# Optimization experiments

Hardware: AMD Instinct MI355X
Metric: run time of the kernel (lower is better)

Reference implementation:

```python
import jax, jax.numpy as jnp
import numpy as np

N_NODES = 50000
N_EDGES = 800000
F_IN = 64
HID = 64
N_GRAPHS = 256
BN_EPS = 1e-5


def setup_inputs() -> dict:
    key = jax.random.key(0)
    ks = jax.random.split(key, 16)
    inp = {
        'x': jax.random.normal(ks[0], (N_NODES, F_IN), dtype=jnp.float32),
        'edge_index': jax.random.randint(ks[1], (2, N_EDGES), 0, N_NODES, dtype=jnp.int64),
        'edge_weight': jax.random.uniform(ks[2], (N_EDGES,), dtype=jnp.float32),
        'batch': jnp.sort(jax.random.randint(ks[3], (N_NODES,), 0, N_GRAPHS, dtype=jnp.int64)),
    }
    def lin(k, fi, fo):
        s = 1.0 / np.sqrt(fi)
        kw, kb = jax.random.split(k)
        return (jax.random.uniform(kw, (fi, fo), jnp.float32, -s, s),
                jax.random.uniform(kb, (fo,), jnp.float32, -s, s))
    inp['W1'], inp['b1'] = lin(ks[4], F_IN, HID)
    inp['W2'], inp['b2'] = lin(ks[5], HID, HID)
    inp['W3'], inp['b3'] = lin(ks[6], HID, HID)
    inp['fcW1'], inp['fcb1'] = lin(ks[7], HID, HID)
    inp['fcW2'], inp['fcb2'] = lin(ks[8], HID, 1)
    for i, k in zip((1, 2, 3), ks[9:12]):
        inp[f'g{i}'] = jnp.ones((HID,), jnp.float32)
        inp[f'be{i}'] = jnp.zeros((HID,), jnp.float32)
    return inp


def gin_conv(x, src, dst, edge_weight, W, b):
    # weighted scatter-add aggregation: agg[dst] += w_e * x[src]
    msg = x[src] * edge_weight[:, None]            # [E, d]
    agg = jax.ops.segment_sum(msg, dst, num_segments=x.shape[0])  # [N, d]
    return (x + agg) @ W + b                       # GIN eps=0, nn = Linear


def batch_norm(x, gamma, beta):
    mu = jnp.mean(x, axis=0)
    var = jnp.var(x, axis=0)
    return (x - mu) * jax.lax.rsqrt(var + BN_EPS) * gamma + beta


def reference(x, edge_index, edge_weight, batch,
              W1, b1, W2, b2, W3, b3, fcW1, fcb1, fcW2, fcb2,
              g1, be1, g2, be2, g3, be3):
    src, dst = edge_index[0], edge_index[1]
    h = batch_norm(jax.nn.relu(gin_conv(x, src, dst, edge_weight, W1, b1)), g1, be1)
    h = batch_norm(jax.nn.relu(gin_conv(h, src, dst, edge_weight, W2, b2)), g2, be2)
    h = batch_norm(gin_conv(h, src, dst, edge_weight, W3, b3), g3, be3)
    pooled = jax.ops.segment_sum(h, batch, num_segments=N_GRAPHS)  # global_add_pool
    h = jax.nn.relu(pooled)
    h = jax.nn.relu(h @ fcW1 + fcb1)
    # dropout is identity in eval / deterministic reference
    return (h @ fcW2 + fcb2).reshape(-1)
```

## Files before the change

### kernel.cpp

```cpp
#include <hip/hip_runtime.h>
#include <hip/hip_bf16.h>


#define NN 50000
#define NE 800000
#define FD 64
#define NG 256
#define CAP 64
#define BN_EPS 1e-5f

__device__ __forceinline__ float4 dec4(uint2 a) {
    float4 f;
    f.x = __uint_as_float(a.x << 16);
    f.y = __uint_as_float(a.x & 0xFFFF0000u);
    f.z = __uint_as_float(a.y << 16);
    f.w = __uint_as_float(a.y & 0xFFFF0000u);
    return f;
}
__device__ __forceinline__ unsigned rbf(float f) {
    unsigned u = __float_as_uint(f);
    return (u + 0x7FFFu + ((u >> 16) & 1u)) >> 16;
}
__device__ __forceinline__ uint2 enc4(float4 v) {
    uint2 o;
    o.x = rbf(v.x) | (rbf(v.y) << 16);
    o.y = rbf(v.z) | (rbf(v.w) << 16);
    return o;
}

__global__ __launch_bounds__(256) void build_slots_kernel(
    const int* __restrict__ src, const int* __restrict__ dst,
    const float* __restrict__ ew, int* __restrict__ cursor,
    unsigned* __restrict__ slots)
{
    int e = blockIdx.x * 256 + threadIdx.x;
    if (e < NE) {
        int d = dst[e];
        int pos = atomicAdd(&cursor[d], 1) & (CAP - 1);
        slots[(size_t)d * CAP + pos] =
            ((unsigned)src[e] << 16) | rbf(ew[e]);
    }
}

__global__ __launch_bounds__(256) void cvt_kernel(
    const float4* __restrict__ xin, uint2* __restrict__ xout)
{
    int i = blockIdx.x * 256 + threadIdx.x;
    xout[i] = enc4(xin[i]);
}

__global__ __launch_bounds__(256) void agg_layer_kernel(
    const uint2* __restrict__ h, const int* __restrict__ deg,
    const unsigned* __restrict__ slots, const float* __restrict__ affine,
    const float* __restrict__ W, const float* __restrict__ b,
    uint2* __restrict__ y, float* __restrict__ buckets, int relu_flag)
{
    __shared__ float Ws[FD * FD];
    __shared__ float ps1[4][FD];
    __shared__ float ps2[4][FD];
    int tid  = threadIdx.x;
    int wave = tid >> 6, lane = tid & 63;
    int g = lane >> 4, l = lane & 15;
    int node = blockIdx.x * 4 + wave;

    {
        float4* Wv = (float4*)Ws;
        const float4* Wg = (const float4*)W;
        #pragma unroll
        for (int i = 0; i < 4; i++) Wv[tid + 256 * i] = Wg[tid + 256 * i];
    }

    unsigned ms = slots[(size_t)node * CAP + lane];
    int dg = deg[node];
    float4 self = dec4(h[(size_t)node * 16 + l]);
    if (dg > CAP) dg = CAP;

    __syncthreads();

    float4 acc = make_float4(0.f, 0.f, 0.f, 0.f);
    float wsum = 0.f;
    int nIter = (dg + 7) >> 3;
    for (int i = 0; i < nIter; i++) {
        int e0 = 8 * i + g;
        int e1 = e0 + 4;
        int ee0 = (e0 < dg) ? e0 : 0;
        int ee1 = (e1 < dg) ? e1 : 0;
        unsigned m0 = (unsigned)__shfl((int)ms, ee0, 64);
        unsigned m1 = (unsigned)__shfl((int)ms, ee1, 64);
        float w0 = __uint_as_float((m0 & 0xFFFFu) << 16);
        float w1 = __uint_as_float((m1 & 0xFFFFu) << 16);
        w0 = (e0 < dg) ? w0 : 0.f;
        w1 = (e1 < dg) ? w1 : 0.f;
        float4 v0 = dec4(h[(size_t)(m0 >> 16) * 16 + l]);
        float4 v1 = dec4(h[(size_t)(m1 >> 16) * 16 + l]);
        wsum += w0 + w1;
        acc.x = fmaf(w0, v0.x, acc.x); acc.y = fmaf(w0, v0.y, acc.y);
        acc.z = fmaf(w0, v0.z, acc.z); acc.w = fmaf(w0, v0.w, acc.w);
        acc.x = fmaf(w1, v1.x, acc.x); acc.y = fmaf(w1, v1.y, acc.y);
        acc.z = fmaf(w1, v1.z, acc.z); acc.w = fmaf(w1, v1.w, acc.w);
    }
    acc.x += __shfl_xor(acc.x, 16, 64); acc.y += __shfl_xor(acc.y, 16, 64);
    acc.z += __shfl_xor(acc.z, 16, 64); acc.w += __shfl_xor(acc.w, 16, 64);
    wsum  += __shfl_xor(wsum, 16, 64);
    acc.x += __shfl_xor(acc.x, 32, 64); acc.y += __shfl_xor(acc.y, 32, 64);
    acc.z += __shfl_xor(acc.z, 32, 64); acc.w += __shfl_xor(acc.w, 32, 64);
    wsum  += __shfl_xor(wsum, 32, 64);

    float4 raw;
    raw.x = self.x + acc.x; raw.y = self.y + acc.y;
    raw.z = self.z + acc.z; raw.w = self.w + acc.w;

    float4 af = make_float4(1.f, 1.f, 1.f, 1.f);
    float4 cf = make_float4(0.f, 0.f, 0.f, 0.f);
    if (affine) {
        af = ((const float4*)affine)[l];
        cf = ((const float4*)(affine + FD))[l];
    }
    float sw = 1.0f + wsum;
    float4 hin;
    hin.x = fmaf(af.x, raw.x, cf.x * sw);
    hin.y = fmaf(af.y, raw.y, cf.y * sw);
    hin.z = fmaf(af.z, raw.z, cf.z * sw);
    hin.w = fmaf(af.w, raw.w, cf.w * sw);

    const float4* __restrict__ WsV = (const float4*)Ws;
    float4 yp = make_float4(0.f, 0.f, 0.f, 0.f);
    #pragma unroll
    for (int kk = 0; kk < 4; kk++) {
        int srcl = 4 * g + kk;
        float a0 = __shfl(hin.x, srcl, 64);
        float a1 = __shfl(hin.y, srcl, 64);
        float a2 = __shfl(hin.z, srcl, 64);
        float a3 = __shfl(hin.w, srcl, 64);
        int k0 = 16 * g + 4 * kk;
        float4 w0 = WsV[(k0 + 0) * 16 + l];
        float4 w1 = WsV[(k0 + 1) * 16 + l];
        float4 w2 = WsV[(k0 + 2) * 16 + l];
        float4 w3 = WsV[(k0 + 3) * 16 + l];
        yp.x = fmaf(a0, w0.x, yp.x); yp.y = fmaf(a0, w0.y, yp.y);
        yp.z = fmaf(a0, w0.z, yp.z); yp.w = fmaf(a0, w0.w, yp.w);
        yp.x = fmaf(a1, w1.x, yp.x); yp.y = fmaf(a1, w1.y, yp.y);
        yp.z = fmaf(a1, w1.z, yp.z); yp.w = fmaf(a1, w1.w, yp.w);
        yp.x = fmaf(a2, w2.x, yp.x); yp.y = fmaf(a2, w2.y, yp.y);
        yp.z = fmaf(a2, w2.z, yp.z); yp.w = fmaf(a2, w2.w, yp.w);
        yp.x = fmaf(a3, w3.x, yp.x); yp.y = fmaf(a3, w3.y, yp.y);
        yp.z = fmaf(a3, w3.z, yp.z); yp.w = fmaf(a3, w3.w, yp.w);
    }
    yp.x += __shfl_xor(yp.x, 16, 64); yp.y += __shfl_xor(yp.y, 16, 64);
    yp.z += __shfl_xor(yp.z, 16, 64); yp.w += __shfl_xor(yp.w, 16, 64);
    yp.x += __shfl_xor(yp.x, 32, 64); yp.y += __shfl_xor(yp.y, 32, 64);
    yp.z += __shfl_xor(yp.z, 32, 64); yp.w += __shfl_xor(yp.w, 32, 64);

    float4 bias = ((const float4*)b)[l];
    float4 yv;
    yv.x = yp.x + bias.x; yv.y = yp.y + bias.y;
    yv.z = yp.z + bias.z; yv.w = yp.w + bias.w;
    if (relu_flag) {
        yv.x = fmaxf(yv.x, 0.f); yv.y = fmaxf(yv.y, 0.f);
        yv.z = fmaxf(yv.z, 0.f); yv.w = fmaxf(yv.w, 0.f);
    }
    if (g == 0) {
        y[(size_t)node * 16 + l] = enc4(yv);
        ((float4*)&ps1[wave][0])[l] = yv;
        float4 sq;
        sq.x = yv.x * yv.x; sq.y = yv.y * yv.y;
        sq.z = yv.z * yv.z; sq.w = yv.w * yv.w;
        ((float4*)&ps2[wave][0])[l] = sq;
    }
    __syncthreads();
    if (tid < FD) {
        float a = ps1[0][tid] + ps1[1][tid] + ps1[2][tid] + ps1[3][tid];
        float q = ps2[0][tid] + ps2[1][tid] + ps2[2][tid] + ps2[3][tid];
        float* bk = buckets + (blockIdx.x & 63) * 128;
        atomicAdd(&bk[tid], a);
        atomicAdd(&bk[FD + tid], q);
    }
}

__global__ __launch_bounds__(256) void finalize_kernel(
    const float* __restrict__ buckets, const float* __restrict__ gamma,
    const float* __restrict__ beta, float* __restrict__ affine)
{
    __shared__ float part[4][2][FD];
    int tid = threadIdx.x;
    int f = tid & 63, q = tid >> 6;
    float S1 = 0.f, S2 = 0.f;
    #pragma unroll
    for (int i = 0; i < 16; i++) {
        int bkt = q * 16 + i;
        S1 += buckets[bkt * 128 + f];
        S2 += buckets[bkt * 128 + FD + f];
    }
    part[q][0][f] = S1;
    part[q][1][f] = S2;
    __syncthreads();
    if (tid < FD) {
        float s1 = part[0][0][tid] + part[1][0][tid] + part[2][0][tid] + part[3][0][tid];
        float s2 = part[0][1][tid] + part[1][1][tid] + part[2][1][tid] + part[3][1][tid];
        float mu  = s1 * (1.f / NN);
        float var = s2 * (1.f / NN) - mu * mu;
        float a = gamma[tid] * rsqrtf(var + BN_EPS);
        affine[tid]      = a;
        affine[FD + tid] = beta[tid] - mu * a;
    }
}

__global__ __launch_bounds__(256) void pool_head_kernel(
    const uint2* __restrict__ y, const int* __restrict__ batch,
    const float* __restrict__ affine3,
    const float* __restrict__ fcW1, const float* __restrict__ fcb1,
    const float* __restrict__ fcW2, const float* __restrict__ fcb2,
    float* __restrict__ out)
{
    __shared__ float red[16][FD];
    __shared__ int bounds[2];
    int tid = threadIdx.x;
    int g = blockIdx.x;
    if (tid < 2) {
        int target = g + tid;
        int lo = 0, hi = NN;
        while (lo < hi) {
            int mid = (lo + hi) >> 1;
            if (batch[mid] < target) lo = mid + 1; else hi = mid;
        }
        bounds[tid] = lo;
    }
    __syncthreads();
    int s = bounds[0], e = bounds[1];
    int l = tid & 15, r = tid >> 4;
    float4 acc = make_float4(0.f, 0.f, 0.f, 0.f);
    for (int n = s + r; n < e; n += 16) {
        float4 v = dec4(y[(size_t)n * 16 + l]);
        acc.x += v.x; acc.y += v.y; acc.z += v.z; acc.w += v.w;
    }
    ((float4*)&red[r][0])[l] = acc;
    __syncthreads();
    for (int off = 8; off > 0; off >>= 1) {
        if (r < off) {
            float4 a = ((float4*)&red[r][0])[l];
            float4 o = ((float4*)&red[r + off][0])[l];
            a.x += o.x; a.y += o.y; a.z += o.z; a.w += o.w;
            ((float4*)&red[r][0])[l] = a;
        }
        __syncthreads();
    }
    if (tid < 64) {
        float cnt = (float)(e - s);
        float p = red[0][tid];
        p = fmaf(affine3[tid], p, affine3[FD + tid] * cnt);
        p = fmaxf(p, 0.f);
        float acc1 = fcb1[tid];
        #pragma unroll
        for (int k = 0; k < FD; k++) {
            float pk = __shfl(p, k, 64);
            acc1 = fmaf(pk, fcW1[k * FD + tid], acc1);
        }
        acc1 = fmaxf(acc1, 0.f);
        float prod = acc1 * fcW2[tid];
        #pragma unroll
        for (int off = 32; off > 0; off >>= 1)
            prod += __shfl_xor(prod, off, 64);
        if (tid == 0) out[g] = prod + fcb2[0];
    }
}

extern "C" void kernel_launch(void* const* d_in, const int* in_sizes, int n_in,
                              void* d_out, int out_size, void* d_ws, size_t ws_size,
                              hipStream_t stream) {
    const float* x     = (const float*)d_in[0];
    const int*   ei    = (const int*)d_in[1];
    const float* ew    = (const float*)d_in[2];
    const int*   batch = (const int*)d_in[3];
    const float* W1 = (const float*)d_in[4],  *b1 = (const float*)d_in[5];
    const float* W2 = (const float*)d_in[6],  *b2 = (const float*)d_in[7];
    const float* W3 = (const float*)d_in[8],  *b3 = (const float*)d_in[9];
    const float* fcW1 = (const float*)d_in[10], *fcb1 = (const float*)d_in[11];
    const float* fcW2 = (const float*)d_in[12], *fcb2 = (const float*)d_in[13];
    const float* g1 = (const float*)d_in[14], *be1 = (const float*)d_in[15];
    const float* g2 = (const float*)d_in[16], *be2 = (const float*)d_in[17];
    const float* g3 = (const float*)d_in[18], *be3 = (const float*)d_in[19];
    float* out = (float*)d_out;

    const int* srcp = ei;
    const int* dstp = ei + NE;

    char* ws = (char*)d_ws;
    size_t off = 0;
    auto take = [&](size_t bytes) -> char* {
        char* p = ws + off;
        off += (bytes + 255) & ~(size_t)255;
        return p;
    };
    uint2*    xbf   = (uint2*)   take((size_t)NN * FD * 2);
    uint2*    bufA  = (uint2*)   take((size_t)NN * FD * 2);
    uint2*    bufB  = (uint2*)   take((size_t)NN * FD * 2);
    unsigned* slots = (unsigned*)take((size_t)NN * CAP * 4);
    float*    affine= (float*)   take((size_t)3 * 2 * FD * 4);
    size_t zero_base = off;
    int*      cursor= (int*)     take((size_t)NN * 4);
    float*    buckets=(float*)   take((size_t)3 * 64 * 128 * 4);
    size_t zero_bytes = off - zero_base;
    (void)ws_size; (void)n_in; (void)in_sizes; (void)out_size;

    hipMemsetAsync(ws + zero_base, 0, zero_bytes, stream);

    build_slots_kernel<<<(NE + 255) / 256, 256, 0, stream>>>(srcp, dstp, ew,
                                                             cursor, slots);
    cvt_kernel<<<(NN * 16) / 256, 256, 0, stream>>>((const float4*)x, xbf);

    const int gridA = NN / 4;

    float* bk1 = buckets + 0 * 64 * 128;
    float* bk2 = buckets + 1 * 64 * 128;
    float* bk3 = buckets + 2 * 64 * 128;
    float* af1 = affine + 0 * 128;
    float* af2 = affine + 1 * 128;
    float* af3 = affine + 2 * 128;

    agg_layer_kernel<<<gridA, 256, 0, stream>>>(xbf, cursor, slots,
                                                nullptr, W1, b1, bufA, bk1, 1);
    finalize_kernel<<<1, 256, 0, stream>>>(bk1, g1, be1, af1);
    agg_layer_kernel<<<gridA, 256, 0, stream>>>(bufA, cursor, slots,
                                                af1, W2, b2, bufB, bk2, 1);
    finalize_kernel<<<1, 256, 0, stream>>>(bk2, g2, be2, af2);
    agg_layer_kernel<<<gridA, 256, 0, stream>>>(bufB, cursor, slots,
                                                af2, W3, b3, bufA, bk3, 0);
    finalize_kernel<<<1, 256, 0, stream>>>(bk3, g3, be3, af3);
    pool_head_kernel<<<NG, 256, 0, stream>>>(bufA, batch, af3,
                                             fcW1, fcb1, fcW2, fcb2, out);
}
```

Baseline: 287.8 us.

## Fuse slot build with bf16 convert, partition scatter by destination, unroll gather

Merges the edge-slot build and the x-to-bf16 conversion into one launch. The build now has each edge chunk read by 8 blocks, and each block only writes edges whose destination falls in its node partition, so atomics and slot writes stay within a narrower address range per block. The aggregation loop handles 16 edges per iteration instead of 8, with four independent gathers in flight to raise memory-level parallelism. The cost is that edge arrays are read eight times over, and the wider unroll adds register pressure.

After: 265.3 us. 7.8% less time.

```diff
diff --git a/kernel.cpp b/kernel.cpp
--- a/kernel.cpp
+++ b/kernel.cpp
@@ -8,6 +8,13 @@
 #define NG 256
 #define CAP 64
 #define BN_EPS 1e-5f
+
+#define NPART 8
+#define PSIZE 6250
+#define ECHUNK 2048
+#define NCHUNK ((NE + ECHUNK - 1) / ECHUNK)
+#define NBUILD (NCHUNK * NPART)
+#define NCVT   ((NN * 16) / 256)
 
 __device__ __forceinline__ float4 dec4(uint2 a) {
     float4 f;
@@ -28,25 +35,34 @@
     return o;
 }
 
-__global__ __launch_bounds__(256) void build_slots_kernel(
+__global__ __launch_bounds__(256) void build_cvt_kernel(
     const int* __restrict__ src, const int* __restrict__ dst,
     const float* __restrict__ ew, int* __restrict__ cursor,
-    unsigned* __restrict__ slots)
-{
-    int e = blockIdx.x * 256 + threadIdx.x;
-    if (e < NE) {
-        int d = dst[e];
-        int pos = atomicAdd(&cursor[d], 1) & (CAP - 1);
-        slots[(size_t)d * CAP + pos] =
-            ((unsigned)src[e] << 16) | rbf(ew[e]);
-    }
-}
-
-__global__ __launch_bounds__(256) void cvt_kernel(
+    unsigned* __restrict__ slots,
     const float4* __restrict__ xin, uint2* __restrict__ xout)
 {
-    int i = blockIdx.x * 256 + threadIdx.x;
-    xout[i] = enc4(xin[i]);
+    int bid = blockIdx.x;
+    int tid = threadIdx.x;
+    if (bid < NBUILD) {
+        int part  = bid & 7;
+        int chunk = bid >> 3;
+        int base  = chunk * ECHUNK;
+        #pragma unroll
+        for (int i = 0; i < ECHUNK; i += 256) {
+            int e = base + i + tid;
+            if (e < NE) {
+                int d = dst[e];
+                if (d / PSIZE == part) {
+                    int pos = atomicAdd(&cursor[d], 1) & (CAP - 1);
+                    slots[(size_t)d * CAP + pos] =
+                        ((unsigned)src[e] << 16) | rbf(ew[e]);
+                }
+            }
+        }
+    } else {
+        int i = (bid - NBUILD) * 256 + tid;
+        xout[i] = enc4(xin[i]);
+    }
 }
 
 __global__ __launch_bounds__(256) void agg_layer_kernel(
@@ -79,25 +95,40 @@
 
     float4 acc = make_float4(0.f, 0.f, 0.f, 0.f);
     float wsum = 0.f;
-    int nIter = (dg + 7) >> 3;
+    int nIter = (dg + 15) >> 4;
     for (int i = 0; i < nIter; i++) {
-        int e0 = 8 * i + g;
-        int e1 = e0 + 4;
+        int e0 = 16 * i + g;
+        int e1 = e0 + 4, e2 = e0 + 8, e3 = e0 + 12;
         int ee0 = (e0 < dg) ? e0 : 0;
         int ee1 = (e1 < dg) ? e1 : 0;
+        int ee2 = (e2 < dg) ? e2 : 0;
+        int ee3 = (e3 < dg) ? e3 : 0;
         unsigned m0 = (unsigned)__shfl((int)ms, ee0, 64);
         unsigned m1 = (unsigned)__shfl((int)ms, ee1, 64);
+        unsigned m2 = (unsigned)__shfl((int)ms, ee2, 64);
+        unsigned m3 = (unsigned)__shfl((int)ms, ee3, 64);
         float w0 = __uint_as_float((m0 & 0xFFFFu) << 16);
         float w1 = __uint_as_float((m1 & 0xFFFFu) << 16);
+        float w2 = __uint_as_float((m2 & 0xFFFFu) << 16);
+        float w3 = __uint_as_float((m3 & 0xFFFFu) << 16);
         w0 = (e0 < dg) ? w0 : 0.f;
         w1 = (e1 < dg) ? w1 : 0.f;
-        float4 v0 = dec4(h[(size_t)(m0 >> 16) * 16 + l]);
-        float4 v1 = dec4(h[(size_t)(m1 >> 16) * 16 + l]);
-        wsum += w0 + w1;
+        w2 = (e2 < dg) ? w2 : 0.f;
+        w3 = (e3 < dg) ? w3 : 0.f;
+        uint2 r0 = h[(size_t)(m0 >> 16) * 16 + l];
+        uint2 r1 = h[(size_t)(m1 >> 16) * 16 + l];
+        uint2 r2 = h[(size_t)(m2 >> 16) * 16 + l];
+        uint2 r3 = h[(size_t)(m3 >> 16) * 16 + l];
+        float4 v0 = dec4(r0), v1 = dec4(r1), v2 = dec4(r2), v3 = dec4(r3);
+        wsum += (w0 + w1) + (w2 + w3);
         acc.x = fmaf(w0, v0.x, acc.x); acc.y = fmaf(w0, v0.y, acc.y);
         acc.z = fmaf(w0, v0.z, acc.z); acc.w = fmaf(w0, v0.w, acc.w);
         acc.x = fmaf(w1, v1.x, acc.x); acc.y = fmaf(w1, v1.y, acc.y);
         acc.z = fmaf(w1, v1.z, acc.z); acc.w = fmaf(w1, v1.w, acc.w);
+        acc.x = fmaf(w2, v2.x, acc.x); acc.y = fmaf(w2, v2.y, acc.y);
+        acc.z = fmaf(w2, v2.z, acc.z); acc.w = fmaf(w2, v2.w, acc.w);
+        acc.x = fmaf(w3, v3.x, acc.x); acc.y = fmaf(w3, v3.y, acc.y);
+        acc.z = fmaf(w3, v3.z, acc.z); acc.w = fmaf(w3, v3.w, acc.w);
     }
     acc.x += __shfl_xor(acc.x, 16, 64); acc.y += __shfl_xor(acc.y, 16, 64);
     acc.z += __shfl_xor(acc.z, 16, 64); acc.w += __shfl_xor(acc.w, 16, 64);
@@ -304,9 +335,9 @@
 
     hipMemsetAsync(ws + zero_base, 0, zero_bytes, stream);
 
-    build_slots_kernel<<<(NE + 255) / 256, 256, 0, stream>>>(srcp, dstp, ew,
-                                                             cursor, slots);
-    cvt_kernel<<<(NN * 16) / 256, 256, 0, stream>>>((const float4*)x, xbf);
+    build_cvt_kernel<<<NBUILD + NCVT, 256, 0, stream>>>(srcp, dstp, ew,
+                                                        cursor, slots,
+                                                        (const float4*)x, xbf);
 
     const int gridA = NN / 4;
 
```
